# Performance work log

Measured on AMD Instinct MI355X. Metric: run time of the kernel, lower is better.

The kernel has to match this reference:

```python
import jax, jax.numpy as jnp
import numpy as np

B, N, E, D = 8, 2048, 4096, 256
HOPS = 3

def setup_inputs() -> dict:
    key = jax.random.key(0)
    ks = jax.random.split(key, 12)
    p = lambda k, shp: (jax.random.normal(k, shp, dtype=jnp.float32) * 0.02)
    return {
        "node_vec": jax.random.normal(ks[0], (B, N, D), dtype=jnp.float32),
        "edge_vec": jax.random.normal(ks[1], (B, E, D), dtype=jnp.float32),
        "node2edge": jax.random.uniform(ks[2], (B, E, N), dtype=jnp.float32),
        "edge2node": jax.random.uniform(ks[3], (B, N, E), dtype=jnp.float32),
        "node_mask": jnp.ones((B, N), dtype=jnp.float32),
        "W_fuse": p(ks[4], (D, 2 * D)), "b_fuse": jnp.zeros((D,), jnp.float32),
        "W_z": p(ks[5], (D, 4 * D)), "b_z": jnp.zeros((D,), jnp.float32),
        "W_update": p(ks[6], (D, 2 * D)),
        "W_reset": p(ks[7], (D, 2 * D)),
        "W_memory": p(ks[8], (D, 2 * D)),
        "W_max": p(ks[9], (D, D)),
    }

def _gnn_step(node_vec, edge_vec, n2e, e2n, W_fuse, b_fuse):
    # n2e: [B,E,N], e2n: [B,N,E]
    edge_emb = jnp.einsum('ben,bnd->bed', n2e, node_vec)          # [B,E,D]
    edge_emb = jax.nn.relu(jnp.concatenate([edge_emb, edge_vec], axis=-1) @ W_fuse.T + b_fuse)
    norm = jnp.sum(e2n, axis=2, keepdims=True) + 1.0               # [B,N,1]
    return (jnp.einsum('bne,bed->bnd', e2n, edge_emb) + node_vec) / norm

def _gated_fusion(in_vec, out_vec, W_z, b_z):
    feats = jnp.concatenate([in_vec, out_vec, in_vec * out_vec, in_vec - out_vec], axis=-1)
    z = jax.nn.sigmoid(feats @ W_z.T + b_z)
    return (1.0 - z) * in_vec + z * out_vec

def _gru_step(cur, new, W_u, W_r, W_m):
    cn = jnp.concatenate([cur, new], axis=-1)
    u = jax.nn.sigmoid(cn @ W_u.T)
    r = jax.nn.sigmoid(cn @ W_r.T)
    m = jnp.tanh(jnp.concatenate([r * cur, new], axis=-1) @ W_m.T)
    return (1.0 - u) * cur + u * m

def reference(node_vec, edge_vec, node2edge, edge2node, node_mask,
              W_fuse, b_fuse, W_z, b_z, W_update, W_reset, W_memory, W_max):
    n2e_T = jnp.swapaxes(node2edge, 1, 2)  # [B,N,E]
    e2n_T = jnp.swapaxes(edge2node, 1, 2)  # [B,E,N]
    for _ in range(HOPS):
        out_vec = _gnn_step(node_vec, edge_vec, node2edge, edge2node, W_fuse, b_fuse)
        in_vec = _gnn_step(node_vec, edge_vec, e2n_T, n2e_T, W_fuse, b_fuse)
        new_vec = _gated_fusion(in_vec, out_vec, W_z, b_z)
        node_vec = _gru_step(node_vec, new_vec, W_update, W_reset, W_memory)
    # graph max-pooling: linear then max over nodes (node_mask unused, as in original)
    graph_embedding = jnp.max(node_vec @ W_max.T, axis=1)          # [B,D]
    return (jnp.swapaxes(node_vec, 0, 1), graph_embedding[None])    # [N,B,D], [1,B,D]
```

## Files before the change

kernel.cpp:

```cpp
#include <hip/hip_runtime.h>
#include <math.h>

#define Bb 8
#define Nn 2048
#define Ee 4096
#define Dd 256
#define HOPS 3

typedef __attribute__((ext_vector_type(4))) float f32x4;
typedef _Float16 f16;
typedef __attribute__((ext_vector_type(8))) _Float16 f16x8;
typedef __attribute__((ext_vector_type(4))) _Float16 f16x4;
typedef __attribute__((ext_vector_type(8))) short s16x8;
typedef __attribute__((ext_vector_type(4))) short s16x4;

__device__ __forceinline__ short f2bf(float f){
  union{float f; unsigned u;} x; x.f=f;
  unsigned r = (x.u + 0x7fffu + ((x.u>>16)&1u)) >> 16;
  return (short)r;
}
__device__ __forceinline__ float bf2f(short h){
  union{unsigned u; float f;} x; x.u = ((unsigned)(unsigned short)h) << 16; return x.f;
}
__device__ __forceinline__ int swz(int row, int idx){ return idx ^ ((row & 7) << 3); }

enum { HN=0, HT=1 };
enum { OF=0, OH=1, OHT=2 };
enum { EP_NONE=0, EP_BIAS, EP_ADDRELUH, EP_AGG };
enum { SM_CN=0, SM_G4, SM_RC };
enum { SE_GATE=0, SE_SIG, SE_TANH };

template<int AMODE, bool AH, int SPL, int EPI, int OUTM>
__global__ __launch_bounds__(512) void hgemm(
    const void* __restrict__ Av, const f16* __restrict__ Bh, void* __restrict__ Cv,
    const float* __restrict__ aux1, const float* __restrict__ aux2,
    const float* __restrict__ bias,
    int M, int Nd, int K, int lda, int ldb, int ldc,
    long sA, long sB, long sC, long sAux1, long sAux2,
    long aLo, long bLo, int maskB, int mask1)
{
  const int bz = blockIdx.z;
  const char* Ab = (const char*)Av + (AH ? bz * sA * 2 : bz * sA * 4);
  Bh += (long)(bz & maskB) * sB;
  char* Cb = (char*)Cv + ((OUTM == OF) ? bz * sC * 4 : bz * sC * 2);
  if (aux1) aux1 += (long)(bz & mask1) * sAux1;
  if (aux2) aux2 += bz * sAux2;
  const int m0 = blockIdx.y * 128;
  const int n0 = blockIdx.x * 128;

  constexpr int HLA = 128 * 64;
  constexpr int HLB = 128 * 64;
  __shared__ f16 As[128 * 64 * ((SPL & 2) ? 2 : 1)];
  __shared__ f16 Bs[128 * 64 * ((SPL & 1) ? 2 : 1)];

  const int tid = threadIdx.x;
  const int wid = tid >> 6, lane = tid & 63;
  const int wm = (wid >> 1) * 32, wn = (wid & 1) * 64;
  const int r = lane & 15, g = lane >> 4;

  f32x4 acc[2][4];
  #pragma unroll
  for (int i = 0; i < 2; i++)
    #pragma unroll
    for (int j = 0; j < 4; j++) acc[i][j] = (f32x4){0.f, 0.f, 0.f, 0.f};

  f16x8 ra0, ra1, rl0, rl1;
  f16x8 rb0, rb1, rbl0, rbl1;

  auto loadA = [&](int k0) {
    if (AMODE == HN && AH) {
      const f16* Ah = (const f16*)Ab;
      const int row = tid >> 2, kc = (tid & 3) * 16;
      const long off = (long)(m0 + row) * lda + k0 + kc;
      ra0 = *(const f16x8*)&Ah[off];
      ra1 = *(const f16x8*)&Ah[off + 8];
      if (SPL & 2) { rl0 = *(const f16x8*)&Ah[aLo + off]; rl1 = *(const f16x8*)&Ah[aLo + off + 8]; }
    } else if (AMODE == HN && !AH) {
      const float* Af = (const float*)Ab;
      const int row = tid >> 2, kc = (tid & 3) * 16;
      const float* s = &Af[(long)(m0 + row) * lda + k0 + kc];
      f32x4 v0 = *(const f32x4*)s,       v1 = *(const f32x4*)(s + 4);
      f32x4 v2 = *(const f32x4*)(s + 8), v3 = *(const f32x4*)(s + 12);
      ra0 = (f16x8){(f16)v0.x,(f16)v0.y,(f16)v0.z,(f16)v0.w,(f16)v1.x,(f16)v1.y,(f16)v1.z,(f16)v1.w};
      ra1 = (f16x8){(f16)v2.x,(f16)v2.y,(f16)v2.z,(f16)v2.w,(f16)v3.x,(f16)v3.y,(f16)v3.z,(f16)v3.w};
    } else {
      const int mm = tid & 127, kh = (tid >> 7) * 16;
      if (AH) {
        const f16* s = &((const f16*)Ab)[(long)(k0 + kh) * lda + m0 + mm];
        #pragma unroll
        for (int j = 0; j < 8; j++) ra0[j] = s[(long)j * lda];
        #pragma unroll
        for (int j = 0; j < 8; j++) ra1[j] = s[(long)(j + 8) * lda];
      } else {
        const float* s = &((const float*)Ab)[(long)(k0 + kh) * lda + m0 + mm];
        #pragma unroll
        for (int j = 0; j < 8; j++) ra0[j] = (f16)s[(long)j * lda];
        #pragma unroll
        for (int j = 0; j < 8; j++) ra1[j] = (f16)s[(long)(j + 8) * lda];
      }
    }
  };
  auto storeA = [&]() {
    if (AMODE == HT) {
      const int mm = tid & 127, kh = (tid >> 7) * 16;
      *(f16x8*)&As[swz(mm, mm * 64 + kh)]     = ra0;
      *(f16x8*)&As[swz(mm, mm * 64 + kh + 8)] = ra1;
    } else {
      const int row = tid >> 2, kc = (tid & 3) * 16;
      const int i0 = swz(row, row * 64 + kc), i1 = swz(row, row * 64 + kc + 8);
      *(f16x8*)&As[i0] = ra0;
      *(f16x8*)&As[i1] = ra1;
      if (SPL & 2) { *(f16x8*)&As[HLA + i0] = rl0; *(f16x8*)&As[HLA + i1] = rl1; }
    }
  };
  auto loadB = [&](int k0) {
    const int row = tid >> 2, kc = (tid & 3) * 16;
    const long off = (long)(n0 + row) * ldb + k0 + kc;
    rb0 = *(const f16x8*)&Bh[off];
    rb1 = *(const f16x8*)&Bh[off + 8];
    if (SPL & 1) { rbl0 = *(const f16x8*)&Bh[bLo + off]; rbl1 = *(const f16x8*)&Bh[bLo + off + 8]; }
  };
  auto storeB = [&]() {
    const int row = tid >> 2, kc = (tid & 3) * 16;
    const int i0 = swz(row, row * 64 + kc), i1 = swz(row, row * 64 + kc + 8);
    *(f16x8*)&Bs[i0] = rb0;
    *(f16x8*)&Bs[i1] = rb1;
    if (SPL & 1) { *(f16x8*)&Bs[HLB + i0] = rbl0; *(f16x8*)&Bs[HLB + i1] = rbl1; }
  };

  loadA(0); loadB(0);
  storeA(); storeB();
  __syncthreads();

  const int NT = K >> 6;
  for (int t = 0; t < NT; t++) {
    const bool more = (t + 1 < NT);
    if (more) { loadA((t + 1) << 6); loadB((t + 1) << 6); }
    #pragma unroll
    for (int ks = 0; ks < 2; ks++) {
      f16x8 af[2], bf[4], afl[2], bfl[4];
      #pragma unroll
      for (int i = 0; i < 2; i++) {
        const int rw = wm + i * 16 + r;
        const int ix = swz(rw, rw * 64 + ks * 32 + g * 8);
        af[i] = *(const f16x8*)&As[ix];
        if (SPL & 2) afl[i] = *(const f16x8*)&As[HLA + ix];
      }
      #pragma unroll
      for (int j = 0; j < 4; j++) {
        const int rw = wn + j * 16 + r;
        const int ix = swz(rw, rw * 64 + ks * 32 + g * 8);
        bf[j] = *(const f16x8*)&Bs[ix];
        if (SPL & 1) bfl[j] = *(const f16x8*)&Bs[HLB + ix];
      }
      #pragma unroll
      for (int i = 0; i < 2; i++)
        #pragma unroll
        for (int j = 0; j < 4; j++) {
          acc[i][j] = __builtin_amdgcn_mfma_f32_16x16x32_f16(af[i], bf[j], acc[i][j], 0, 0, 0);
          if (SPL & 1)
            acc[i][j] = __builtin_amdgcn_mfma_f32_16x16x32_f16(af[i], bfl[j], acc[i][j], 0, 0, 0);
          if (SPL & 2)
            acc[i][j] = __builtin_amdgcn_mfma_f32_16x16x32_f16(afl[i], bf[j], acc[i][j], 0, 0, 0);
        }
    }
    __syncthreads();
    if (more) { storeA(); storeB(); __syncthreads(); }
  }

  if (OUTM == OHT) {
    f16* tile = (f16*)Bs;
    #pragma unroll
    for (int half = 0; half < 2; half++) {
      __syncthreads();
      if ((wm >> 6) == half) {
        #pragma unroll
        for (int i = 0; i < 2; i++)
          #pragma unroll
          for (int j = 0; j < 4; j++) {
            const int rowl = wm + i * 16 + g * 4 - 64 * half;
            const int coll = wn + j * 16 + r;
            #pragma unroll
            for (int t = 0; t < 4; t++) {
              float v = acc[i][j][t];
              if (EPI == EP_ADDRELUH) {
                v += (float)((const f16*)aux1)[(long)(m0 + 64 * half + rowl + t) * 256 + n0 + coll];
                v = v > 0.f ? v : 0.f;
              } else if (EPI == EP_BIAS) { v += bias[n0 + coll]; }
              tile[coll * 72 + rowl + t] = (f16)v;
            }
          }
      }
      __syncthreads();
      const int c2 = tid >> 2, rs = (tid & 3) * 16;
      f16* dst = &((f16*)Cb)[(long)(n0 + c2) * ldc + m0 + 64 * half + rs];
      *(f16x8*)dst       = *(const f16x8*)&tile[c2 * 72 + rs];
      *(f16x8*)(dst + 8) = *(const f16x8*)&tile[c2 * 72 + rs + 8];
    }
  } else {
    #pragma unroll
    for (int i = 0; i < 2; i++) {
      #pragma unroll
      for (int j = 0; j < 4; j++) {
        const int rowb = m0 + wm + i * 16 + g * 4;
        const int col = n0 + wn + j * 16 + r;
        #pragma unroll
        for (int t = 0; t < 4; t++) {
          const int row = rowb + t;
          const long idx = (long)row * ldc + col;
          float v = acc[i][j][t];
          if (EPI == EP_BIAS)          { v += bias[col]; }
          else if (EPI == EP_ADDRELUH) { v += (float)((const f16*)aux1)[(long)row * 256 + col];
                                         v = v > 0.f ? v : 0.f; }
          else if (EPI == EP_AGG)      { v = (v + aux1[idx]) * aux2[row]; }
          if (OUTM == OH) ((f16*)Cb)[idx] = (f16)v;
          else            ((float*)Cb)[idx] = v;
        }
      }
    }
  }
}

template<int AMODE, int EPI>
__global__ __launch_bounds__(512) void ggemm(
    const float* __restrict__ A, const float* __restrict__ A2, const float* __restrict__ A3,
    const short* __restrict__ Bw, float* __restrict__ C,
    const float* __restrict__ aux1, const float* __restrict__ aux2, const float* __restrict__ bias,
    int Nd, int K, int lda, int ldb, int ldc, long bLo)
{
  const int m0 = blockIdx.y * 128;
  const int n0 = blockIdx.x * 128;
  constexpr int HLA = 128 * 64;
  constexpr int HLB = 128 * 64;
  __shared__ short As[128 * 64 * 2];
  __shared__ short Bs[128 * 64 * 2];

  const int tid = threadIdx.x;
  const int wid = tid >> 6, lane = tid & 63;
  const int wm = (wid >> 1) * 32, wn = (wid & 1) * 64;
  const int r = lane & 15, g = lane >> 4;

  f32x4 acc[2][4];
  #pragma unroll
  for (int i = 0; i < 2; i++)
    #pragma unroll
    for (int j = 0; j < 4; j++) acc[i][j] = (f32x4){0.f, 0.f, 0.f, 0.f};

  s16x4 rah[4], ral[4];
  s16x8 rbh0, rbh1, rbl0, rbl1;

  auto loadA = [&](int k0) {
    const int row = tid >> 2, kc = (tid & 3) * 16;
    const int kk = k0 + kc, q = kk >> 8, kd = kk & 255;
    const long base = (long)(m0 + row) * 256 + kd;
    const long baseA = (long)(m0 + row) * lda + kd;
    #pragma unroll
    for (int u = 0; u < 4; u++) {
      f32x4 v;
      if (AMODE == SM_CN) {
        v = (q == 0) ? *(const f32x4*)(A + base + 4 * u)
                     : *(const f32x4*)(A2 + base + 4 * u);
      } else if (AMODE == SM_G4) {
        if (q == 0)      v = *(const f32x4*)(A  + base + 4 * u);
        else if (q == 1) v = *(const f32x4*)(A2 + base + 4 * u);
        else {
          f32x4 x = *(const f32x4*)(A  + base + 4 * u);
          f32x4 y = *(const f32x4*)(A2 + base + 4 * u);
          v = (q == 2) ? x * y : x - y;
        }
      } else {
        if (q == 0) {
          f32x4 x = *(const f32x4*)(A  + baseA + 4 * u);
          f32x4 y = *(const f32x4*)(A2 + base + 4 * u);
          v = x * y;
        } else v = *(const f32x4*)(A3 + base + 4 * u);
      }
      s16x4 h = { f2bf(v.x), f2bf(v.y), f2bf(v.z), f2bf(v.w) };
      rah[u] = h;
      ral[u] = (s16x4){ f2bf(v.x - bf2f(h.x)), f2bf(v.y - bf2f(h.y)),
                        f2bf(v.z - bf2f(h.z)), f2bf(v.w - bf2f(h.w)) };
    }
  };
  auto storeA = [&]() {
    const int row = tid >> 2, kc = (tid & 3) * 16;
    const int i0 = swz(row, row * 64 + kc), i1 = swz(row, row * 64 + kc + 8);
    *(s16x4*)&As[i0]     = rah[0]; *(s16x4*)&As[i0 + 4] = rah[1];
    *(s16x4*)&As[i1]     = rah[2]; *(s16x4*)&As[i1 + 4] = rah[3];
    *(s16x4*)&As[HLA + i0]     = ral[0]; *(s16x4*)&As[HLA + i0 + 4] = ral[1];
    *(s16x4*)&As[HLA + i1]     = ral[2]; *(s16x4*)&As[HLA + i1 + 4] = ral[3];
  };
  auto loadB = [&](int k0) {
    const int row = tid >> 2, kc = (tid & 3) * 16;
    const long off = (long)(n0 + row) * ldb + k0 + kc;
    rbh0 = *(const s16x8*)&Bw[off];
    rbh1 = *(const s16x8*)&Bw[off + 8];
    rbl0 = *(const s16x8*)&Bw[bLo + off];
    rbl1 = *(const s16x8*)&Bw[bLo + off + 8];
  };
  auto storeB = [&]() {
    const int row = tid >> 2, kc = (tid & 3) * 16;
    const int i0 = swz(row, row * 64 + kc), i1 = swz(row, row * 64 + kc + 8);
    *(s16x8*)&Bs[i0] = rbh0;
    *(s16x8*)&Bs[i1] = rbh1;
    *(s16x8*)&Bs[HLB + i0] = rbl0;
    *(s16x8*)&Bs[HLB + i1] = rbl1;
  };

  loadA(0); loadB(0);
  storeA(); storeB();
  __syncthreads();

  const int NT = K >> 6;
  for (int t = 0; t < NT; t++) {
    const bool more = (t + 1 < NT);
    if (more) { loadA((t + 1) << 6); loadB((t + 1) << 6); }
    #pragma unroll
    for (int ks = 0; ks < 2; ks++) {
      s16x8 ah[2], al[2], bh[4], bl[4];
      #pragma unroll
      for (int i = 0; i < 2; i++) {
        const int rw = wm + i * 16 + r;
        const int ix = swz(rw, rw * 64 + ks * 32 + g * 8);
        ah[i] = *(const s16x8*)&As[ix];
        al[i] = *(const s16x8*)&As[HLA + ix];
      }
      #pragma unroll
      for (int j = 0; j < 4; j++) {
        const int rw = wn + j * 16 + r;
        const int ix = swz(rw, rw * 64 + ks * 32 + g * 8);
        bh[j] = *(const s16x8*)&Bs[ix];
        bl[j] = *(const s16x8*)&Bs[HLB + ix];
      }
      #pragma unroll
      for (int i = 0; i < 2; i++)
        #pragma unroll
        for (int j = 0; j < 4; j++) {
          acc[i][j] = __builtin_amdgcn_mfma_f32_16x16x32_bf16(ah[i], bh[j], acc[i][j], 0, 0, 0);
          acc[i][j] = __builtin_amdgcn_mfma_f32_16x16x32_bf16(ah[i], bl[j], acc[i][j], 0, 0, 0);
          acc[i][j] = __builtin_amdgcn_mfma_f32_16x16x32_bf16(al[i], bh[j], acc[i][j], 0, 0, 0);
        }
    }
    __syncthreads();
    if (more) { storeA(); storeB(); __syncthreads(); }
  }

  #pragma unroll
  for (int i = 0; i < 2; i++) {
    #pragma unroll
    for (int j = 0; j < 4; j++) {
      #pragma unroll
      for (int t = 0; t < 4; t++) {
        const int row = m0 + wm + i * 16 + g * 4 + t;
        const int col = n0 + wn + j * 16 + r;
        float v = acc[i][j][t];
        if (EPI == SE_GATE) {
          v += bias[col];
          float z = 1.f / (1.f + __expf(-v));
          const long ix = (long)row * 256 + col;
          v = (1.f - z) * aux1[ix] + z * aux2[ix];
        } else if (EPI == SE_SIG) {
          v = 1.f / (1.f + __expf(-v));
        } else {
          v = tanhf(v);
        }
        C[(long)row * ldc + col] = v;
      }
    }
  }
}


template<bool SUMDST>
__global__ void cvt_dual(const float* __restrict__ in, f16* __restrict__ outR,
                         f16* __restrict__ outT, float* __restrict__ part, int R, int C) {
  __shared__ f16 t[64][72];
  __shared__ float sacc[64][4];
  const long boff = (long)blockIdx.z * (long)R * C;
  const int r0 = blockIdx.x * 64, c0 = blockIdx.y * 64;
  const int tid = threadIdx.x;
  const int rl = tid >> 2, cl = (tid & 3) * 16;
  const float* src = in + boff + (long)(r0 + rl) * C + c0 + cl;
  f16 loc[16];
  float s = 0.f;
  #pragma unroll
  for (int u = 0; u < 4; u++) {
    f32x4 v = *(const f32x4*)(src + 4 * u);
    loc[4*u+0] = (f16)v.x; loc[4*u+1] = (f16)v.y; loc[4*u+2] = (f16)v.z; loc[4*u+3] = (f16)v.w;
    if (!SUMDST) s += v.x + v.y + v.z + v.w;
  }
  f16* dR = outR + boff + (long)(r0 + rl) * C + c0 + cl;
  *(f16x8*)dR       = *(const f16x8*)&loc[0];
  *(f16x8*)(dR + 8) = *(const f16x8*)&loc[8];
  *(f16x8*)&t[rl][cl]     = *(const f16x8*)&loc[0];
  *(f16x8*)&t[rl][cl + 8] = *(const f16x8*)&loc[8];
  if (!SUMDST) sacc[rl][tid & 3] = s;
  __syncthreads();
  const int cl2 = tid >> 2, rl2 = (tid & 3) * 16;
  f16x8 o0, o1;
  #pragma unroll
  for (int v = 0; v < 8; v++) { o0[v] = t[rl2 + v][cl2]; o1[v] = t[rl2 + 8 + v][cl2]; }
  if (SUMDST) {
    float s2 = 0.f;
    #pragma unroll
    for (int v = 0; v < 8; v++) s2 += (float)o0[v] + (float)o1[v];
    sacc[cl2][tid & 3] = s2;
  }
  f16* dT = outT + boff + (long)(c0 + cl2) * R + r0 + rl2;
  *(f16x8*)dT = o0;
  *(f16x8*)(dT + 8) = o1;
  __syncthreads();
  if (tid < 64) {
    float tot = sacc[tid][0] + sacc[tid][1] + sacc[tid][2] + sacc[tid][3];
    const int slot = SUMDST ? blockIdx.x : blockIdx.y;
    const int n    = (SUMDST ? c0 : r0) + tid;
    part[((long)blockIdx.z * 64 + slot) * Nn + n] = tot;
  }
}

__global__ void colfin64(const float* __restrict__ part, float* __restrict__ rn) {
  const int i = blockIdx.x * 256 + threadIdx.x;
  const int b = i >> 11, n = i & 2047;
  float s = 0.f;
  for (int c = 0; c < 64; c++) s += part[((long)b * 64 + c) * Nn + n];
  rn[i] = 1.f / (1.f + s);
}

__global__ void rowsum_kernel(const float* __restrict__ e2n, float* __restrict__ out) {
  const int gw = blockIdx.x * 4 + (threadIdx.x >> 6);
  const int lane = threadIdx.x & 63;
  const float* p = e2n + (long)gw * Ee;
  float s = 0.f;
  for (int e = lane; e < Ee; e += 64) s += p[e];
  #pragma unroll
  for (int off = 32; off; off >>= 1) s += __shfl_down(s, off);
  if (lane == 0) out[gw] = 1.f / (1.f + s);
}
__global__ void colsum_kernel(const float* __restrict__ n2e, float* __restrict__ part) {
  const int n = blockIdx.x * 256 + threadIdx.x;
  const int c = blockIdx.y, b = blockIdx.z;
  const float* p = n2e + (long)b * Ee * Nn + (long)c * 256 * Nn + n;
  float s = 0.f;
  for (int e = 0; e < 256; e++) s += p[(long)e * Nn];
  part[((long)b * 16 + c) * Nn + n] = s;
}
__global__ void colfin16(const float* __restrict__ part, float* __restrict__ rni) {
  const int i = blockIdx.x * 256 + threadIdx.x;
  const int b = i >> 11, n = i & 2047;
  float s = 0.f;
  #pragma unroll
  for (int c = 0; c < 16; c++) s += part[((long)b * 16 + c) * Nn + n];
  rni[i] = 1.f / (1.f + s);
}

__global__ void cvt_half(const float* __restrict__ src, f16* __restrict__ dst) {
  const long i4 = (long)blockIdx.x * 256 + threadIdx.x;
  f32x4 v = *(const f32x4*)&src[i4 * 4];
  *(f16x4*)&dst[i4 * 4] = (f16x4){(f16)v.x, (f16)v.y, (f16)v.z, (f16)v.w};
}

__global__ void cvt_half_split(const float* __restrict__ src, f16* __restrict__ dst, long loOff) {
  const long i4 = (long)blockIdx.x * 256 + threadIdx.x;
  f32x4 v = *(const f32x4*)&src[i4 * 4];
  f16x4 h = {(f16)v.x, (f16)v.y, (f16)v.z, (f16)v.w};
  *(f16x4*)&dst[i4 * 4] = h;
  f16x4 l = {(f16)(v.x - (float)h[0]), (f16)(v.y - (float)h[1]),
             (f16)(v.z - (float)h[2]), (f16)(v.w - (float)h[3])};
  *(f16x4*)&dst[loOff + i4 * 4] = l;
}

__global__ void cvt_bf_split(const float* __restrict__ src, short* __restrict__ dst, long loOff) {
  const long i4 = (long)blockIdx.x * 256 + threadIdx.x;
  f32x4 v = *(const f32x4*)&src[i4 * 4];
  s16x4 h = { f2bf(v.x), f2bf(v.y), f2bf(v.z), f2bf(v.w) };
  *(s16x4*)&dst[i4 * 4] = h;
  s16x4 l = { f2bf(v.x - bf2f(h.x)), f2bf(v.y - bf2f(h.y)),
              f2bf(v.z - bf2f(h.z)), f2bf(v.w - bf2f(h.w)) };
  *(s16x4*)&dst[loOff + i4 * 4] = l;
}

__global__ void init_cur(const float* __restrict__ node_vec, float* __restrict__ cur,
                         f16* __restrict__ cur_h, long loOff) {
  const long i4 = (long)blockIdx.x * 256 + threadIdx.x;
  f32x4 v = *(const f32x4*)&node_vec[i4 * 4];
  *(f32x4*)&cur[i4 * 4] = v;
  f16x4 h = {(f16)v.x, (f16)v.y, (f16)v.z, (f16)v.w};
  *(f16x4*)&cur_h[i4 * 4] = h;
  f16x4 l = {(f16)(v.x - (float)h[0]), (f16)(v.y - (float)h[1]),
             (f16)(v.z - (float)h[2]), (f16)(v.w - (float)h[3])};
  *(f16x4*)&cur_h[loOff + i4 * 4] = l;
}

__global__ void transposeT(const float* __restrict__ cur, f16* __restrict__ curT, long loOff) {
  __shared__ f16 th[64][72];
  __shared__ f16 tl[64][72];
  const int b = blockIdx.z, nt = blockIdx.x * 64, dt = blockIdx.y * 64;
  const int tid = threadIdx.x;
  const int nl = tid >> 2, d0 = (tid & 3) * 16;
  const float* src = cur + ((long)b * Nn + nt + nl) * 256 + dt + d0;
  #pragma unroll
  for (int u = 0; u < 4; u++) {
    f32x4 v = *(const f32x4*)(src + 4 * u);
    f16x4 h = {(f16)v.x, (f16)v.y, (f16)v.z, (f16)v.w};
    *(f16x4*)&th[nl][d0 + 4 * u] = h;
    f16x4 l = {(f16)(v.x - (float)h[0]), (f16)(v.y - (float)h[1]),
               (f16)(v.z - (float)h[2]), (f16)(v.w - (float)h[3])};
    *(f16x4*)&tl[nl][d0 + 4 * u] = l;
  }
  __syncthreads();
  const int dl = tid >> 2, n0l = (tid & 3) * 16;
  f16x8 o0, o1, p0, p1;
  #pragma unroll
  for (int v = 0; v < 8; v++) {
    o0[v] = th[n0l + v][dl];     o1[v] = th[n0l + 8 + v][dl];
    p0[v] = tl[n0l + v][dl];     p1[v] = tl[n0l + 8 + v][dl];
  }
  f16* dst = curT + (long)b * (256 * Nn) + (long)(dt + dl) * Nn + nt + n0l;
  *(f16x8*)dst = o0;
  *(f16x8*)(dst + 8) = o1;
  *(f16x8*)(dst + loOff) = p0;
  *(f16x8*)(dst + loOff + 8) = p1;
}

__global__ void gruf_kernel(const float* __restrict__ urb, const float* __restrict__ m,
                            float* __restrict__ cur, f16* __restrict__ cur_h, long loOff) {
  const long i = (long)blockIdx.x * 256 + threadIdx.x;
  const long bn = i >> 8; const int d = i & 255;
  const float uu = urb[bn * 512 + d];
  const float v = (1.f - uu) * cur[i] + uu * m[i];
  cur[i] = v;
  f16 h = (f16)v;
  cur_h[i] = h;
  cur_h[loOff + i] = (f16)(v - (float)h);
}

__global__ void maxpool1(const float* __restrict__ pooled, float* __restrict__ part) {
  const int d = threadIdx.x, c = blockIdx.x, b = blockIdx.y;
  const float* p = pooled + ((long)b * Nn + c * 256) * Dd + d;
  float m = -INFINITY;
  for (int n = 0; n < 256; n++) m = fmaxf(m, p[(long)n * Dd]);
  part[(b * 8 + c) * Dd + d] = m;
}
__global__ void maxpool2(const float* __restrict__ part, float* __restrict__ out1) {
  const int d = threadIdx.x, b = blockIdx.x;
  float m = -INFINITY;
  #pragma unroll
  for (int c = 0; c < 8; c++) m = fmaxf(m, part[(b * 8 + c) * Dd + d]);
  out1[b * Dd + d] = m;
}
__global__ void transpose_out(const float* __restrict__ cur, float* __restrict__ out0) {
  const long i = (long)blockIdx.x * 256 + threadIdx.x;
  const int d = i & 255;
  const long nb = i >> 8;
  const int b = nb & 7;
  const long n = nb >> 3;
  out0[i] = cur[((long)b * Nn + n) * Dd + d];
}

extern "C" void kernel_launch(void* const* d_in, const int* in_sizes, int n_in,
                              void* d_out, int out_size, void* d_ws, size_t ws_size,
                              hipStream_t stream) {
  const float* node_vec = (const float*)d_in[0];
  const float* edge_vec = (const float*)d_in[1];
  const float* n2e      = (const float*)d_in[2];
  const float* e2n      = (const float*)d_in[3];
  const float* W_fuse   = (const float*)d_in[5];
  const float* b_fuse   = (const float*)d_in[6];
  const float* W_z      = (const float*)d_in[7];
  const float* b_z      = (const float*)d_in[8];
  const float* W_u      = (const float*)d_in[9];
  const float* W_r      = (const float*)d_in[10];
  const float* W_m      = (const float*)d_in[11];
  const float* W_max    = (const float*)d_in[12];

  const long ND  = (long)Bb * Nn * Dd;
  const long EDb = (long)Ee * Dd;
  const long NDb = (long)Nn * Dd;
  const long ED  = (long)Bb * EDb;
  const long ADJb = (long)Ee * Nn;
  const long ADJ = (long)Bb * ADJb;
  const int  BN  = Bb * Nn;

  char* p = (char*)d_ws;
  auto alloc = [&](size_t bytes) { char* r = p; p += (bytes + 255) & ~(size_t)255; return r; };

  const size_t need_full =
      (size_t)4 * ADJ * 2
      + (size_t)ED * 2
      + (size_t)4 * ED * 2
      + (size_t)ED * 2
      + (size_t)4 * ND * 2
      + (size_t)(2 * 131072 + 2 * 65536) * 2
      + (size_t)(2 * 262144 + 2 * 262144 + 2 * 131072) * 2
      + (size_t)5 * ND * 4
      + (size_t)BN * 512 * 4
      + (size_t)(2 * BN + 2 * 64 * BN) * 4
      + 64 * 1024;
  const bool full = ws_size >= need_full;

  f16 *adjEO = nullptr, *adjAG = nullptr;
  f16 *n2e_h = nullptr, *e2n_hT = nullptr, *e2n_h = nullptr, *n2e_hT = nullptr;
  if (full) {
    adjEO = (f16*)alloc((size_t)2 * ADJ * 2);
    adjAG = (f16*)alloc((size_t)2 * ADJ * 2);
    n2e_h = adjEO;  e2n_hT = adjEO + ADJ;
    e2n_h = adjAG;  n2e_hT = adjAG + ADJ;
  }
  f16* ev_h    = (f16*)alloc(ED * 2);
  f16* E1h2    = (f16*)alloc((size_t)2 * ED * 2);
  f16* E2T2    = (f16*)alloc((size_t)2 * ED * 2);
  f16* EVWh    = (f16*)alloc(ED * 2);
  f16* cur_h   = (f16*)alloc(2 * ND * 2);
  f16* cur_hT  = (f16*)alloc(2 * ND * 2);
  f16* Wf_h    = (f16*)alloc(2 * 131072 * 2);
  f16* Wmax_h  = (f16*)alloc(2 * 65536 * 2);
  short* Wz_s  = (short*)alloc((size_t)2 * 262144 * 2);
  short* Wur_s = (short*)alloc((size_t)2 * 262144 * 2);
  short* Wm_s  = (short*)alloc((size_t)2 * 131072 * 2);
  float* cur   = (float*)alloc(ND * 4);
  float* outv  = (float*)alloc(2 * ND * 4);
  float* inv   = outv + ND;
  float* nv    = (float*)alloc(ND * 4);
  float* urb   = (float*)alloc((size_t)BN * 512 * 4);
  float* mb    = (float*)alloc(ND * 4);
  float* rno   = (float*)alloc(2 * BN * 4);
  float* rni   = rno + BN;
  float* rnopart = (float*)alloc((size_t)64 * BN * 4);
  float* rnipart = (float*)alloc((size_t)64 * BN * 4);
  float* maxpart = (float*)alloc(BN * 4);

  float* out0 = (float*)d_out;
  float* out1 = out0 + ND;

  if (full) {
    cvt_dual<false><<<dim3(Nn / 64, Ee / 64, Bb), 256, 0, stream>>>(
        e2n, e2n_h, e2n_hT, rnopart, Nn, Ee);
    cvt_dual<true><<<dim3(Ee / 64, Nn / 64, Bb), 256, 0, stream>>>(
        n2e, n2e_h, n2e_hT, rnipart, Ee, Nn);
    colfin64<<<BN / 256, 256, 0, stream>>>(rnopart, rno);
    colfin64<<<BN / 256, 256, 0, stream>>>(rnipart, rni);
  } else {
    colsum_kernel<<<dim3(Nn / 256, 16, Bb), 256, 0, stream>>>(n2e, rnipart);
    colfin16<<<BN / 256, 256, 0, stream>>>(rnipart, rni);
    rowsum_kernel<<<BN / 4, 256, 0, stream>>>(e2n, rno);
  }
  cvt_half<<<(int)(ED / 1024), 256, 0, stream>>>(edge_vec, ev_h);
  cvt_half_split<<<131072 / 1024, 256, 0, stream>>>(W_fuse, Wf_h, 131072);
  cvt_half_split<<<65536 / 1024, 256, 0, stream>>>(W_max, Wmax_h, 65536);
  cvt_bf_split<<<262144 / 1024, 256, 0, stream>>>(W_z, Wz_s, 262144);
  cvt_bf_split<<<131072 / 1024, 256, 0, stream>>>(W_u, Wur_s, 262144);
  cvt_bf_split<<<131072 / 1024, 256, 0, stream>>>(W_r, Wur_s + 131072, 262144);
  cvt_bf_split<<<131072 / 1024, 256, 0, stream>>>(W_m, Wm_s, 131072);
  init_cur<<<(int)(ND / 1024), 256, 0, stream>>>(node_vec, cur, cur_h, ND);
  transposeT<<<dim3(Nn / 64, 4, Bb), 256, 0, stream>>>(cur, cur_hT, ND);

  hgemm<HN, true, 1, EP_BIAS, OH><<<dim3(2, Ee / 128, Bb), 512, 0, stream>>>(
      ev_h, Wf_h + 256, EVWh, nullptr, nullptr, b_fuse,
      Ee, 256, 256, 256, 512, 256, EDb, 0, EDb, 0, 0, 0, 131072, 0, 0);

  for (int h = 0; h < HOPS; h++) {
    if (full) {
      hgemm<HN, true, 1, EP_NONE, OH><<<dim3(2, Ee / 128, 2 * Bb), 512, 0, stream>>>(
          adjEO, cur_hT, E1h2, nullptr, nullptr, nullptr,
          Ee, 256, Nn, Nn, Nn, 256, ADJb, NDb, EDb, 0, 0, 0, ND, 7, 0);
      hgemm<HN, true, 1, EP_ADDRELUH, OHT><<<dim3(2, Ee / 128, 2 * Bb), 512, 0, stream>>>(
          E1h2, Wf_h, E2T2, (const float*)EVWh, nullptr, nullptr,
          Ee, 256, 256, 256, 512, Ee, EDb, 0, EDb, EDb / 2, 0, 0, 131072, 0, 7);
      hgemm<HN, true, 0, EP_AGG, OF><<<dim3(2, Nn / 128, 2 * Bb), 512, 0, stream>>>(
          adjAG, E2T2, outv, cur, rno, nullptr,
          Nn, 256, Ee, Ee, Ee, 256, ADJb, EDb, NDb, NDb, (long)Nn, 0, 0, 15, 7);
    } else {
      hgemm<HN, false, 1, EP_NONE, OH><<<dim3(2, Ee / 128, Bb), 512, 0, stream>>>(
          n2e, cur_hT, E1h2, nullptr, nullptr, nullptr,
          Ee, 256, Nn, Nn, Nn, 256, ADJb, NDb, EDb, 0, 0, 0, ND, 7, 0);
      hgemm<HT, false, 1, EP_NONE, OH><<<dim3(2, Ee / 128, Bb), 512, 0, stream>>>(
          e2n, cur_hT, E1h2 + ED, nullptr, nullptr, nullptr,
          Ee, 256, Nn, Ee, Nn, 256, ADJb, NDb, EDb, 0, 0, 0, ND, 7, 0);
      hgemm<HN, true, 1, EP_ADDRELUH, OHT><<<dim3(2, Ee / 128, 2 * Bb), 512, 0, stream>>>(
          E1h2, Wf_h, E2T2, (const float*)EVWh, nullptr, nullptr,
          Ee, 256, 256, 256, 512, Ee, EDb, 0, EDb, EDb / 2, 0, 0, 131072, 0, 7);
      hgemm<HN, false, 0, EP_AGG, OF><<<dim3(2, Nn / 128, Bb), 512, 0, stream>>>(
          e2n, E2T2, outv, cur, rno, nullptr,
          Nn, 256, Ee, Ee, Ee, 256, (long)Nn * Ee, EDb, NDb, NDb, (long)Nn, 0, 0, 15, 7);
      hgemm<HT, false, 0, EP_AGG, OF><<<dim3(2, Nn / 128, Bb), 512, 0, stream>>>(
          n2e, E2T2 + ED, inv, cur, rni, nullptr,
          Nn, 256, Ee, Nn, Ee, 256, (long)Ee * Nn, EDb, NDb, NDb, (long)Nn, 0, 0, 15, 7);
    }
    ggemm<SM_G4, SE_GATE><<<dim3(2, BN / 128, 1), 512, 0, stream>>>(
        inv, outv, nullptr, Wz_s, nv, inv, outv, b_z, 256, 1024, 256, 1024, 256, 262144);
    ggemm<SM_CN, SE_SIG><<<dim3(4, BN / 128, 1), 512, 0, stream>>>(
        cur, nv, nullptr, Wur_s, urb, nullptr, nullptr, nullptr, 512, 512, 256, 512, 512, 262144);
    ggemm<SM_RC, SE_TANH><<<dim3(2, BN / 128, 1), 512, 0, stream>>>(
        urb + 256, cur, nv, Wm_s, mb, nullptr, nullptr, nullptr, 256, 512, 512, 512, 256, 131072);
    gruf_kernel<<<(int)(ND / 256), 256, 0, stream>>>(urb, mb, cur, cur_h, ND);
    if (h < HOPS - 1)
      transposeT<<<dim3(Nn / 64, 4, Bb), 256, 0, stream>>>(cur, cur_hT, ND);
  }

  hgemm<HN, true, 3, EP_NONE, OF><<<dim3(2, BN / 128, 1), 512, 0, stream>>>(
      cur_h, Wmax_h, urb, nullptr, nullptr, nullptr,
      BN, 256, 256, 256, 256, 256, 0, 0, 0, 0, 0, ND, 65536, 0, 0);
  maxpool1<<<dim3(8, Bb), 256, 0, stream>>>(urb, maxpart);
  maxpool2<<<Bb, 256, 0, stream>>>(maxpart, out1);

  transpose_out<<<(int)(ND / 256), 256, 0, stream>>>(cur, out0);
}
```

Measured before the change: 1.665 ms.

## Use direct global-to-LDS loads for fp16 row-major GEMM and B operand

Replaces the register-staged global→LDS copies with the global_load_lds builtin for the row-major fp16 A/B path of hgemm and for the B operand of the split-bf16 GEMM. The lane-to-address mapping uses an XOR so the data lands in the existing swizzled LDS layout. This removes VGPR staging and ds_write instructions. In exchange the hgemm fast path loses its register prefetch overlap: it now loads, syncs and computes each tile in turn. The bf16 kernel issues B loads after the compute phase, so that copy also no longer overlaps with compute.

```diff
diff --git a/kernel.cpp b/kernel.cpp
--- a/kernel.cpp
+++ b/kernel.cpp
@@ -23,6 +23,12 @@
   union{unsigned u; float f;} x; x.u = ((unsigned)(unsigned short)h) << 16; return x.f;
 }
 __device__ __forceinline__ int swz(int row, int idx){ return idx ^ ((row & 7) << 3); }
+
+typedef const __attribute__((address_space(1))) void cas1_t;
+typedef __attribute__((address_space(3))) void as3_t;
+__device__ __forceinline__ void gl16(const void* g, void* l) {
+  __builtin_amdgcn_global_load_lds((cas1_t*)g, (as3_t*)l, 16, 0, 0);
+}
 
 enum { HN=0, HT=1 };
 enum { OF=0, OH=1, OHT=2 };
@@ -64,78 +70,7 @@
     #pragma unroll
     for (int j = 0; j < 4; j++) acc[i][j] = (f32x4){0.f, 0.f, 0.f, 0.f};
 
-  f16x8 ra0, ra1, rl0, rl1;
-  f16x8 rb0, rb1, rbl0, rbl1;
-
-  auto loadA = [&](int k0) {
-    if (AMODE == HN && AH) {
-      const f16* Ah = (const f16*)Ab;
-      const int row = tid >> 2, kc = (tid & 3) * 16;
-      const long off = (long)(m0 + row) * lda + k0 + kc;
-      ra0 = *(const f16x8*)&Ah[off];
-      ra1 = *(const f16x8*)&Ah[off + 8];
-      if (SPL & 2) { rl0 = *(const f16x8*)&Ah[aLo + off]; rl1 = *(const f16x8*)&Ah[aLo + off + 8]; }
-    } else if (AMODE == HN && !AH) {
-      const float* Af = (const float*)Ab;
-      const int row = tid >> 2, kc = (tid & 3) * 16;
-      const float* s = &Af[(long)(m0 + row) * lda + k0 + kc];
-      f32x4 v0 = *(const f32x4*)s,       v1 = *(const f32x4*)(s + 4);
-      f32x4 v2 = *(const f32x4*)(s + 8), v3 = *(const f32x4*)(s + 12);
-      ra0 = (f16x8){(f16)v0.x,(f16)v0.y,(f16)v0.z,(f16)v0.w,(f16)v1.x,(f16)v1.y,(f16)v1.z,(f16)v1.w};
-      ra1 = (f16x8){(f16)v2.x,(f16)v2.y,(f16)v2.z,(f16)v2.w,(f16)v3.x,(f16)v3.y,(f16)v3.z,(f16)v3.w};
-    } else {
-      const int mm = tid & 127, kh = (tid >> 7) * 16;
-      if (AH) {
-        const f16* s = &((const f16*)Ab)[(long)(k0 + kh) * lda + m0 + mm];
-        #pragma unroll
-        for (int j = 0; j < 8; j++) ra0[j] = s[(long)j * lda];
-        #pragma unroll
-        for (int j = 0; j < 8; j++) ra1[j] = s[(long)(j + 8) * lda];
-      } else {
-        const float* s = &((const float*)Ab)[(long)(k0 + kh) * lda + m0 + mm];
-        #pragma unroll
-        for (int j = 0; j < 8; j++) ra0[j] = (f16)s[(long)j * lda];
-        #pragma unroll
-        for (int j = 0; j < 8; j++) ra1[j] = (f16)s[(long)(j + 8) * lda];
-      }
-    }
-  };
-  auto storeA = [&]() {
-    if (AMODE == HT) {
-      const int mm = tid & 127, kh = (tid >> 7) * 16;
-      *(f16x8*)&As[swz(mm, mm * 64 + kh)]     = ra0;
-      *(f16x8*)&As[swz(mm, mm * 64 + kh + 8)] = ra1;
-    } else {
-      const int row = tid >> 2, kc = (tid & 3) * 16;
-      const int i0 = swz(row, row * 64 + kc), i1 = swz(row, row * 64 + kc + 8);
-      *(f16x8*)&As[i0] = ra0;
-      *(f16x8*)&As[i1] = ra1;
-      if (SPL & 2) { *(f16x8*)&As[HLA + i0] = rl0; *(f16x8*)&As[HLA + i1] = rl1; }
-    }
-  };
-  auto loadB = [&](int k0) {
-    const int row = tid >> 2, kc = (tid & 3) * 16;
-    const long off = (long)(n0 + row) * ldb + k0 + kc;
-    rb0 = *(const f16x8*)&Bh[off];
-    rb1 = *(const f16x8*)&Bh[off + 8];
-    if (SPL & 1) { rbl0 = *(const f16x8*)&Bh[bLo + off]; rbl1 = *(const f16x8*)&Bh[bLo + off + 8]; }
-  };
-  auto storeB = [&]() {
-    const int row = tid >> 2, kc = (tid & 3) * 16;
-    const int i0 = swz(row, row * 64 + kc), i1 = swz(row, row * 64 + kc + 8);
-    *(f16x8*)&Bs[i0] = rb0;
-    *(f16x8*)&Bs[i1] = rb1;
-    if (SPL & 1) { *(f16x8*)&Bs[HLB + i0] = rbl0; *(f16x8*)&Bs[HLB + i1] = rbl1; }
-  };
-
-  loadA(0); loadB(0);
-  storeA(); storeB();
-  __syncthreads();
-
-  const int NT = K >> 6;
-  for (int t = 0; t < NT; t++) {
-    const bool more = (t + 1 < NT);
-    if (more) { loadA((t + 1) << 6); loadB((t + 1) << 6); }
+  auto mfmaPhase = [&]() {
     #pragma unroll
     for (int ks = 0; ks < 2; ks++) {
       f16x8 af[2], bf[4], afl[2], bfl[4];
@@ -164,8 +99,98 @@
             acc[i][j] = __builtin_amdgcn_mfma_f32_16x16x32_f16(afl[i], bf[j], acc[i][j], 0, 0, 0);
         }
     }
+  };
+
+  const int NT = K >> 6;
+
+  if constexpr (AMODE == HN && AH) {
+    const f16* Ah = (const f16*)Ab;
+    const int rsub = lane >> 3;
+    const int gq = (lane & 7) ^ rsub;
+    for (int t = 0; t < NT; t++) {
+      const int k0 = t << 6;
+      #pragma unroll
+      for (int is = 0; is < 2; is++) {
+        const int row = is * 64 + wid * 8 + rsub;
+        const int lofs = is * 4096 + wid * 512;
+        const f16* sa = Ah + (long)(m0 + row) * lda + k0 + gq * 8;
+        gl16(sa, &As[lofs]);
+        if (SPL & 2) gl16(sa + aLo, &As[HLA + lofs]);
+        const f16* sb = Bh + (long)(n0 + row) * ldb + k0 + gq * 8;
+        gl16(sb, &Bs[lofs]);
+        if (SPL & 1) gl16(sb + bLo, &Bs[HLB + lofs]);
+      }
+      __syncthreads();
+      mfmaPhase();
+      __syncthreads();
+    }
+  } else {
+    f16x8 ra0, ra1, rl0, rl1;
+    f16x8 rb0, rb1, rbl0, rbl1;
+
+    auto loadA = [&](int k0) {
+      if (AMODE == HN && !AH) {
+        const float* Af = (const float*)Ab;
+        const int row = tid >> 2, kc = (tid & 3) * 16;
+        const float* s = &Af[(long)(m0 + row) * lda + k0 + kc];
+        f32x4 v0 = *(const f32x4*)s,       v1 = *(const f32x4*)(s + 4);
+        f32x4 v2 = *(const f32x4*)(s + 8), v3 = *(const f32x4*)(s + 12);
+        ra0 = (f16x8){(f16)v0.x,(f16)v0.y,(f16)v0.z,(f16)v0.w,(f16)v1.x,(f16)v1.y,(f16)v1.z,(f16)v1.w};
+        ra1 = (f16x8){(f16)v2.x,(f16)v2.y,(f16)v2.z,(f16)v2.w,(f16)v3.x,(f16)v3.y,(f16)v3.z,(f16)v3.w};
+      } else {
+        const int mm = tid & 127, kh = (tid >> 7) * 16;
+        if (AH) {
+          const f16* s = &((const f16*)Ab)[(long)(k0 + kh) * lda + m0 + mm];
+          #pragma unroll
+          for (int j = 0; j < 8; j++) ra0[j] = s[(long)j * lda];
+          #pragma unroll
+          for (int j = 0; j < 8; j++) ra1[j] = s[(long)(j + 8) * lda];
+        } else {
+          const float* s = &((const float*)Ab)[(long)(k0 + kh) * lda + m0 + mm];
+          #pragma unroll
+          for (int j = 0; j < 8; j++) ra0[j] = (f16)s[(long)j * lda];
+          #pragma unroll
+          for (int j = 0; j < 8; j++) ra1[j] = (f16)s[(long)(j + 8) * lda];
+        }
+      }
+    };
+    auto storeA = [&]() {
+      if (AMODE == HT) {
+        const int mm = tid & 127, kh = (tid >> 7) * 16;
+        *(f16x8*)&As[swz(mm, mm * 64 + kh)]     = ra0;
+        *(f16x8*)&As[swz(mm, mm * 64 + kh + 8)] = ra1;
+      } else {
+        const int row = tid >> 2, kc = (tid & 3) * 16;
+        const int i0 = swz(row, row * 64 + kc), i1 = swz(row, row * 64 + kc + 8);
+        *(f16x8*)&As[i0] = ra0;
+        *(f16x8*)&As[i1] = ra1;
+      }
+    };
+    auto loadB = [&](int k0) {
+      const int row = tid >> 2, kc = (tid & 3) * 16;
+      const long off = (long)(n0 + row) * ldb + k0 + kc;
+      rb0 = *(const f16x8*)&Bh[off];
+      rb1 = *(const f16x8*)&Bh[off + 8];
+      if (SPL & 1) { rbl0 = *(const f16x8*)&Bh[bLo + off]; rbl1 = *(const f16x8*)&Bh[bLo + off + 8]; }
+    };
+    auto storeB = [&]() {
+      const int row = tid >> 2, kc = (tid & 3) * 16;
+      const int i0 = swz(row, row * 64 + kc), i1 = swz(row, row * 64 + kc + 8);
+      *(f16x8*)&Bs[i0] = rb0;
+      *(f16x8*)&Bs[i1] = rb1;
+      if (SPL & 1) { *(f16x8*)&Bs[HLB + i0] = rbl0; *(f16x8*)&Bs[HLB + i1] = rbl1; }
+    };
+
+    loadA(0); loadB(0);
+    storeA(); storeB();
     __syncthreads();
-    if (more) { storeA(); storeB(); __syncthreads(); }
+    for (int t = 0; t < NT; t++) {
+      const bool more = (t + 1 < NT);
+      if (more) { loadA((t + 1) << 6); loadB((t + 1) << 6); }
+      mfmaPhase();
+      __syncthreads();
+      if (more) { storeA(); storeB(); __syncthreads(); }
+    }
   }
 
   if (OUTM == OHT) {
@@ -247,7 +272,6 @@
     for (int j = 0; j < 4; j++) acc[i][j] = (f32x4){0.f, 0.f, 0.f, 0.f};
 
   s16x4 rah[4], ral[4];
-  s16x8 rbh0, rbh1, rbl0, rbl1;
 
   auto loadA = [&](int k0) {
     const int row = tid >> 2, kc = (tid & 3) * 16;
@@ -289,31 +313,28 @@
     *(s16x4*)&As[HLA + i0]     = ral[0]; *(s16x4*)&As[HLA + i0 + 4] = ral[1];
     *(s16x4*)&As[HLA + i1]     = ral[2]; *(s16x4*)&As[HLA + i1 + 4] = ral[3];
   };
-  auto loadB = [&](int k0) {
-    const int row = tid >> 2, kc = (tid & 3) * 16;
-    const long off = (long)(n0 + row) * ldb + k0 + kc;
-    rbh0 = *(const s16x8*)&Bw[off];
-    rbh1 = *(const s16x8*)&Bw[off + 8];
-    rbl0 = *(const s16x8*)&Bw[bLo + off];
-    rbl1 = *(const s16x8*)&Bw[bLo + off + 8];
+  const int rsub = lane >> 3;
+  const int gq = (lane & 7) ^ rsub;
+  auto issueB = [&](int k0) {
+    #pragma unroll
+    for (int is = 0; is < 2; is++) {
+      const int row = is * 64 + wid * 8 + rsub;
+      const int lofs = is * 4096 + wid * 512;
+      const short* sb = Bw + (long)(n0 + row) * ldb + k0 + gq * 8;
+      gl16(sb, &Bs[lofs]);
+      gl16(sb + bLo, &Bs[HLB + lofs]);
+    }
   };
-  auto storeB = [&]() {
-    const int row = tid >> 2, kc = (tid & 3) * 16;
-    const int i0 = swz(row, row * 64 + kc), i1 = swz(row, row * 64 + kc + 8);
-    *(s16x8*)&Bs[i0] = rbh0;
-    *(s16x8*)&Bs[i1] = rbh1;
-    *(s16x8*)&Bs[HLB + i0] = rbl0;
-    *(s16x8*)&Bs[HLB + i1] = rbl1;
-  };
-
-  loadA(0); loadB(0);
-  storeA(); storeB();
+
+  loadA(0);
+  issueB(0);
+  storeA();
   __syncthreads();
 
   const int NT = K >> 6;
   for (int t = 0; t < NT; t++) {
     const bool more = (t + 1 < NT);
-    if (more) { loadA((t + 1) << 6); loadB((t + 1) << 6); }
+    if (more) loadA((t + 1) << 6);
     #pragma unroll
     for (int ks = 0; ks < 2; ks++) {
       s16x8 ah[2], al[2], bh[4], bl[4];
@@ -341,7 +362,7 @@
         }
     }
     __syncthreads();
-    if (more) { storeA(); storeB(); __syncthreads(); }
+    if (more) { issueB((t + 1) << 6); storeA(); __syncthreads(); }
   }
 
   #pragma unroll
```

After: 1.666 ms. Within noise of the previous version (+0.1%).
